# Optimization experiments

Measured on AMD Instinct MI355X. Metric: run time of the kernel, lower is better.

Reference implementation:

```python
import jax, jax.numpy as jnp
import numpy as np

EMBED_DIM = 384
HEADS = 6
HEAD_DIM = EMBED_DIM // HEADS
WINDOW = 64
B, T, M = 256, 256, 128


def setup_inputs() -> dict:
    key = jax.random.key(0)
    ks = jax.random.split(key, 7)
    s = 0.02
    return {
        "x": jax.random.normal(ks[0], (B, T, EMBED_DIM), dtype=jnp.float32),
        "memory": jax.random.normal(ks[1], (M, EMBED_DIM), dtype=jnp.float32),
        "loss_mask": jnp.ones((B, T), dtype=jnp.float32),
        "qkv_w": jax.random.normal(ks[2], (3 * EMBED_DIM, EMBED_DIM), dtype=jnp.float32) * s,
        "qkv_b": jnp.zeros((3 * EMBED_DIM,), dtype=jnp.float32),
        "proj_w": jax.random.normal(ks[3], (EMBED_DIM, EMBED_DIM), dtype=jnp.float32) * s,
        "proj_b": jnp.zeros((EMBED_DIM,), dtype=jnp.float32),
        "gate": jnp.ones((EMBED_DIM,), dtype=jnp.float32),
    }


def reference(x, memory, loss_mask, qkv_w, qkv_b, proj_w, proj_b, gate):
    Bb, Tt, C = x.shape
    H, D, W = HEADS, HEAD_DIM, WINDOW
    Mm = memory.shape[0]
    T_total = Mm + Tt

    qkv = x @ qkv_w.T + qkv_b                     # [B, T, 3C]
    q, k, v = jnp.split(qkv, 3, axis=-1)
    mem = jnp.broadcast_to(memory[None], (Bb, Mm, C))
    k = jnp.concatenate([mem, k], axis=1)          # [B, M+T, C]
    v = jnp.concatenate([mem, v], axis=1)

    q = q.reshape(Bb, Tt, H, D)
    k = k.reshape(Bb, T_total, H, D)
    v = v.reshape(Bb, T_total, H, D)

    att = jnp.einsum('bthd,bshd->bhts', q, k) * (1.0 / np.sqrt(D))  # [B,H,T,M+T]

    # memory prefix columns are fully attended; self-block is causal AND local-window
    i = jnp.arange(Tt)[:, None]
    j = jnp.arange(Tt)[None, :]
    self_mask = (j <= i) & (jnp.abs(i - j) <= W)   # [T, T]
    full_mask = jnp.concatenate(
        [jnp.ones((Tt, Mm), dtype=bool), self_mask], axis=1)  # [T, M+T]
    att = jnp.where(full_mask[None, None], att, -jnp.inf)
    att = jax.nn.softmax(att, axis=-1)

    out = jnp.einsum('bhts,bshd->bthd', att, v).reshape(Bb, Tt, C)
    out = (out * gate) @ proj_w.T + proj_b
    out = out * loss_mask[..., None]
    return out
```

## Files before the change

### kernel.cpp

```cpp
#include <hip/hip_runtime.h>
#include <hip/hip_bf16.h>

#define Bb 256
#define Tt 256
#define Cc 384
#define Hh 6
#define Dd 64
#define Ww 64
#define Mm 128

typedef short short8 __attribute__((ext_vector_type(8)));
typedef float floatx4 __attribute__((ext_vector_type(4)));

static __device__ __forceinline__ unsigned short f2bf(float f) {
  union { __hip_bfloat16 h; unsigned short u; } cvt;
  cvt.h = __float2bfloat16(f);
  return cvt.u;
}

static __device__ __forceinline__ void gl2lds16(const unsigned short* g, unsigned short* l) {
  __builtin_amdgcn_global_load_lds(
      (const __attribute__((address_space(1))) unsigned int*)(const void*)g,
      (__attribute__((address_space(3))) unsigned int*)(void*)l,
      16, 0, 0);
}


__global__ __launch_bounds__(256) void cvt_x(const float4* __restrict__ x,
                                             ushort4* __restrict__ xb) {
  size_t i = (size_t)blockIdx.x * 256 + threadIdx.x;
  float4 v = x[i];
  ushort4 o;
  o.x = f2bf(v.x); o.y = f2bf(v.y); o.z = f2bf(v.z); o.w = f2bf(v.w);
  xb[i] = o;
}

__global__ __launch_bounds__(256) void cvt_misc(const float* __restrict__ qkv_w,
                                                const float* __restrict__ proj_w,
                                                const float* __restrict__ mem,
                                                unsigned short* __restrict__ wb,
                                                unsigned short* __restrict__ pwb,
                                                unsigned short* __restrict__ memk,
                                                unsigned short* __restrict__ memvt) {
  int i = blockIdx.x * 256 + threadIdx.x;
  wb[i] = f2bf(qkv_w[i]);
  if (i < 147456) pwb[i] = f2bf(proj_w[i]);
  if (i < 49152) {
    int m = i / Cc, c = i % Cc, h = c >> 6, d = c & 63;
    unsigned short bv = f2bf(mem[i]);
    memk[(h * Mm + m) * Dd + d] = bv;
    memvt[(h * Dd + d) * Mm + m] = bv;
  }
}


__global__ __launch_bounds__(256) void gemm_qkv(const unsigned short* __restrict__ xb,
                                                const unsigned short* __restrict__ wb,
                                                const float* __restrict__ qkv_b,
                                                unsigned short* __restrict__ q,
                                                unsigned short* __restrict__ k,
                                                unsigned short* __restrict__ vt)
{
  int tid = threadIdx.x;
  int w = tid >> 6, lane = tid & 63, quad = lane >> 4, l16 = lane & 15;

  int orig = blockIdx.y * 9 + blockIdx.x;
  int newid = (orig & 7) * 576 + (orig >> 3);
  int bx = newid % 9, by = newid / 9;

  int rowbase = by * 128;
  int colbase = bx * 128;
  int rowofs = (w >> 1) * 64, colofs = (w & 1) * 64;

  __shared__ __align__(16) unsigned short Alds[2][128 * 32];
  __shared__ __align__(16) unsigned short Blds[2][128 * 32];

  int srow = lane >> 2;
  int skc = (lane & 3) * 8;

#define STAGE_QKV(buf, ks_) do {                                                  \
    int kk = (ks_) * 32;                                                          \
    _Pragma("unroll")                                                             \
    for (int c = w; c < 8; c += 4) {                                              \
      gl2lds16(xb + (size_t)(rowbase + c * 16 + srow) * 384 + kk + skc,           \
               &Alds[buf][c * 512 + lane * 8]);                                   \
      gl2lds16(wb + (size_t)(colbase + c * 16 + srow) * 384 + kk + skc,           \
               &Blds[buf][c * 512 + lane * 8]);                                   \
    }                                                                             \
  } while (0)

#define COMPUTE_QKV(buf) do {                                                     \
    short8 a[4], b[4];                                                            \
    _Pragma("unroll")                                                             \
    for (int rt = 0; rt < 4; ++rt)                                                \
      a[rt] = *reinterpret_cast<const short8*>(                                   \
          &Alds[buf][(rowofs + rt * 16 + l16) * 32 + quad * 8]);                  \
    _Pragma("unroll")                                                             \
    for (int nt = 0; nt < 4; ++nt)                                                \
      b[nt] = *reinterpret_cast<const short8*>(                                   \
          &Blds[buf][(colofs + nt * 16 + l16) * 32 + quad * 8]);                  \
    _Pragma("unroll")                                                             \
    for (int rt = 0; rt < 4; ++rt)                                                \
      _Pragma("unroll")                                                           \
      for (int nt = 0; nt < 4; ++nt)                                              \
        acc[rt][nt] = __builtin_amdgcn_mfma_f32_16x16x32_bf16(a[rt], b[nt],       \
                                                              acc[rt][nt], 0, 0, 0); \
  } while (0)

  floatx4 acc[4][4] = {};
  STAGE_QKV(0, 0);
  __syncthreads();
#pragma unroll
  for (int ks = 0; ks < 12; ks += 2) {
    STAGE_QKV(1, ks + 1);
    COMPUTE_QKV(0);
    __syncthreads();
    if (ks + 2 < 12) STAGE_QKV(0, ks + 2);
    COMPUTE_QKV(1);
    __syncthreads();
  }

#pragma unroll
  for (int nt = 0; nt < 4; ++nt) {
    int col = colbase + colofs + nt * 16 + l16;
    int which = col >= 768 ? 2 : (col >= 384 ? 1 : 0);
    int cc = col - which * 384;
    int h = cc >> 6, d = cc & 63;
    float bias = qkv_b[col];
#pragma unroll
    for (int rt = 0; rt < 4; ++rt) {
#pragma unroll
      for (int r = 0; r < 4; ++r) {
        int row = rowbase + rowofs + rt * 16 + quad * 4 + r;
        int bidx = row >> 8, t = row & 255;
        float val = acc[rt][nt][r] + bias;
        size_t bh = (size_t)bidx * Hh + h;
        if (which == 0) {
          q[(bh * Tt + t) * Dd + d] = f2bf(val * 0.125f);
        } else if (which == 1) {
          k[(bh * Tt + t) * Dd + d] = f2bf(val);
        } else {
          vt[(bh * Dd + d) * Tt + t] = f2bf(val);
        }
      }
    }
  }
#undef STAGE_QKV
#undef COMPUTE_QKV
}

#define PSTRIDE 264

__global__ __launch_bounds__(256, 2) void attn(const unsigned short* __restrict__ q,
                                               const unsigned short* __restrict__ k,
                                               const unsigned short* __restrict__ vt,
                                               const unsigned short* __restrict__ memk,
                                               const unsigned short* __restrict__ memvt,
                                               const float* __restrict__ gate,
                                               unsigned short* __restrict__ aout)
{
  int tq = blockIdx.x, h = blockIdx.y, b = blockIdx.z;
  int t0 = tq * 64;
  int tid = threadIdx.x, w = tid >> 6, lane = tid & 63, quad = lane >> 4, l16 = lane & 15;

  size_t bh = (size_t)b * Hh + h;
  const unsigned short* qp = q + (bh * Tt + t0 + w * 16) * Dd;
  const unsigned short* kp = k + bh * Tt * Dd;
  const unsigned short* vp = vt + bh * Dd * Tt;
  const unsigned short* mkp = memk + (size_t)h * Mm * Dd;
  const unsigned short* mvp = memvt + (size_t)h * Dd * Mm;

  __shared__ __align__(16) unsigned short lds[33280];
  unsigned short* Kmem = lds;
  unsigned short* Kwin = lds + 8192;
  unsigned short* Pb   = lds;
  unsigned short* Vmem = lds + 16896;
  unsigned short* Vwin = lds + 25088;
  unsigned short* pw = Pb + w * 16 * PSTRIDE;

  short8 qa[2];
#pragma unroll
  for (int ks = 0; ks < 2; ++ks)
    qa[ks] = *reinterpret_cast<const short8*>(qp + l16 * Dd + ks * 32 + quad * 8);

#pragma unroll
  for (int i = 0; i < 4; ++i) {
    int G = (i * 4 + w) * 64;
    int g = G + lane;
    int r = g >> 3, cs = g & 7;
    int c = cs ^ (r & 7);
    gl2lds16(mkp + r * 64 + c * 8, Kmem + G * 8 + lane * 8);
  }
#pragma unroll
  for (int i = 0; i < 4; ++i) {
    int G = (i * 4 + w) * 64;
    int g = G + lane;
    int r = g >> 3, cs = g & 7;
    int c = cs ^ (r & 7);
    int j = t0 - 64 + r;
    if (j < 0) j = 0;
    gl2lds16(kp + (size_t)j * 64 + c * 8, Kwin + G * 8 + lane * 8);
  }
#pragma unroll
  for (int i = 0; i < 4; ++i) {
    int G = (i * 4 + w) * 64;
    int g = G + lane;
    int d = g >> 4, cs = g & 15;
    int c = (cs & 8) | ((cs & 7) ^ (d & 7));
    gl2lds16(mvp + d * Mm + c * 8, Vmem + G * 8 + lane * 8);
  }
#pragma unroll
  for (int i = 0; i < 4; ++i) {
    int G = (i * 4 + w) * 64;
    int g = G + lane;
    int d = g >> 4, cs = g & 15;
    int c = (cs & 8) | ((cs & 7) ^ (d & 7));
    int j0 = t0 - 64 + c * 8;
    if (j0 < 0) j0 = 0;
    gl2lds16(vp + (size_t)d * Tt + j0, Vwin + G * 8 + lane * 8);
  }
  __syncthreads();

  floatx4 s[16] = {};

#pragma unroll
  for (int ct = 0; ct < 8; ++ct)
#pragma unroll
    for (int ks = 0; ks < 2; ++ks) {
      int slot = (ks * 4 + quad) ^ (l16 & 7);
      short8 bf = *reinterpret_cast<const short8*>(Kmem + (ct * 16 + l16) * 64 + slot * 8);
      s[ct] = __builtin_amdgcn_mfma_f32_16x16x32_bf16(qa[ks], bf, s[ct], 0, 0, 0);
    }
#pragma unroll
  for (int ct = 0; ct < 8; ++ct) {
    if (ct >= w && ct <= w + 4) {
#pragma unroll
      for (int ks = 0; ks < 2; ++ks) {
        int slot = (ks * 4 + quad) ^ (l16 & 7);
        short8 bf = *reinterpret_cast<const short8*>(Kwin + (ct * 16 + l16) * 64 + slot * 8);
        s[8 + ct] = __builtin_amdgcn_mfma_f32_16x16x32_bf16(qa[ks], bf, s[8 + ct], 0, 0, 0);
      }
    }
  }
  __syncthreads();

#pragma unroll
  for (int ct = 8; ct < 16; ++ct) {
    int j = t0 - 64 + (ct - 8) * 16 + l16;
#pragma unroll
    for (int r = 0; r < 4; ++r) {
      int i = t0 + w * 16 + quad * 4 + r;
      bool valid = (j >= 0) && (j <= i) && (i - j <= 64);
      if (!valid) s[ct][r] = -1e30f;
    }
  }

  float rm[4], rs[4], inv[4];
#pragma unroll
  for (int r = 0; r < 4; ++r) {
    float m = -1e30f;
#pragma unroll
    for (int ct = 0; ct < 16; ++ct) m = fmaxf(m, s[ct][r]);
    rm[r] = m;
  }
#pragma unroll
  for (int off = 1; off < 16; off <<= 1)
#pragma unroll
    for (int r = 0; r < 4; ++r) rm[r] = fmaxf(rm[r], __shfl_xor(rm[r], off, 64));
#pragma unroll
  for (int r = 0; r < 4; ++r) {
    float sum = 0.f;
#pragma unroll
    for (int ct = 0; ct < 16; ++ct) {
      float p = __expf(s[ct][r] - rm[r]);
      s[ct][r] = p;
      sum += p;
    }
    rs[r] = sum;
  }
#pragma unroll
  for (int off = 1; off < 16; off <<= 1)
#pragma unroll
    for (int r = 0; r < 4; ++r) rs[r] += __shfl_xor(rs[r], off, 64);
#pragma unroll
  for (int r = 0; r < 4; ++r) inv[r] = 1.0f / rs[r];

#pragma unroll
  for (int ct = 0; ct < 16; ++ct)
#pragma unroll
    for (int r = 0; r < 4; ++r)
      pw[(quad * 4 + r) * PSTRIDE + ct * 16 + l16] = f2bf(s[ct][r]);

  floatx4 o[4] = {};
#pragma unroll
  for (int ks = 0; ks < 4; ++ks) {
    short8 pa = *reinterpret_cast<const short8*>(pw + l16 * PSTRIDE + ks * 32 + quad * 8);
#pragma unroll
    for (int dt = 0; dt < 4; ++dt) {
      int c0 = ks * 4 + quad;
      int slot = (c0 & 8) | ((c0 & 7) ^ (l16 & 7));
      short8 vb = *reinterpret_cast<const short8*>(Vmem + (dt * 16 + l16) * 128 + slot * 8);
      o[dt] = __builtin_amdgcn_mfma_f32_16x16x32_bf16(pa, vb, o[dt], 0, 0, 0);
    }
  }
#pragma unroll
  for (int ks = 0; ks < 4; ++ks) {
    if (ks >= (w >> 1) && ks <= 2 + (w >> 1)) {
      short8 pa = *reinterpret_cast<const short8*>(pw + l16 * PSTRIDE + (4 + ks) * 32 + quad * 8);
#pragma unroll
      for (int dt = 0; dt < 4; ++dt) {
        int c0 = ks * 4 + quad;
        int slot = (c0 & 8) | ((c0 & 7) ^ (l16 & 7));
        short8 vb = *reinterpret_cast<const short8*>(Vwin + (dt * 16 + l16) * 128 + slot * 8);
        o[dt] = __builtin_amdgcn_mfma_f32_16x16x32_bf16(pa, vb, o[dt], 0, 0, 0);
      }
    }
  }

#pragma unroll
  for (int dt = 0; dt < 4; ++dt) {
    int c = h * 64 + dt * 16 + l16;
    float g = gate[c];
#pragma unroll
    for (int r = 0; r < 4; ++r) {
      int t = t0 + w * 16 + quad * 4 + r;
      float val = o[dt][r] * inv[r] * g;
      aout[((size_t)b * Tt + t) * Cc + c] = f2bf(val);
    }
  }
}


__global__ __launch_bounds__(256) void gemm_proj(const unsigned short* __restrict__ ab,
                                                 const unsigned short* __restrict__ pwb,
                                                 const float* __restrict__ proj_b,
                                                 const float* __restrict__ loss_mask,
                                                 float* __restrict__ out)
{
  int tid = threadIdx.x;
  int w = tid >> 6, lane = tid & 63, quad = lane >> 4, l16 = lane & 15;

  int orig = blockIdx.y * 3 + blockIdx.x;
  int newid = (orig & 7) * 192 + (orig >> 3);
  int bx = newid % 3, by = newid / 3;

  int rowbase = by * 128;
  int colbase = bx * 128;
  int rowofs = (w >> 1) * 64, colofs = (w & 1) * 64;

  __shared__ __align__(16) unsigned short Alds[2][128 * 32];
  __shared__ __align__(16) unsigned short Blds[2][128 * 32];

  int srow = lane >> 2;
  int skc = (lane & 3) * 8;

#define STAGE_PROJ(buf, ks_) do {                                                 \
    int kk = (ks_) * 32;                                                          \
    _Pragma("unroll")                                                             \
    for (int c = w; c < 8; c += 4) {                                              \
      gl2lds16(ab + (size_t)(rowbase + c * 16 + srow) * 384 + kk + skc,           \
               &Alds[buf][c * 512 + lane * 8]);                                   \
      gl2lds16(pwb + (size_t)(colbase + c * 16 + srow) * 384 + kk + skc,          \
               &Blds[buf][c * 512 + lane * 8]);                                   \
    }                                                                             \
  } while (0)

#define COMPUTE_PROJ(buf) do {                                                    \
    short8 a[4], b[4];                                                            \
    _Pragma("unroll")                                                             \
    for (int rt = 0; rt < 4; ++rt)                                                \
      a[rt] = *reinterpret_cast<const short8*>(                                   \
          &Alds[buf][(rowofs + rt * 16 + l16) * 32 + quad * 8]);                  \
    _Pragma("unroll")                                                             \
    for (int nt = 0; nt < 4; ++nt)                                                \
      b[nt] = *reinterpret_cast<const short8*>(                                   \
          &Blds[buf][(colofs + nt * 16 + l16) * 32 + quad * 8]);                  \
    _Pragma("unroll")                                                             \
    for (int rt = 0; rt < 4; ++rt)                                                \
      _Pragma("unroll")                                                           \
      for (int nt = 0; nt < 4; ++nt)                                              \
        acc[rt][nt] = __builtin_amdgcn_mfma_f32_16x16x32_bf16(a[rt], b[nt],       \
                                                              acc[rt][nt], 0, 0, 0); \
  } while (0)

  floatx4 acc[4][4] = {};
  STAGE_PROJ(0, 0);
  __syncthreads();
#pragma unroll
  for (int ks = 0; ks < 12; ks += 2) {
    STAGE_PROJ(1, ks + 1);
    COMPUTE_PROJ(0);
    __syncthreads();
    if (ks + 2 < 12) STAGE_PROJ(0, ks + 2);
    COMPUTE_PROJ(1);
    __syncthreads();
  }

#pragma unroll
  for (int nt = 0; nt < 4; ++nt) {
    int col = colbase + colofs + nt * 16 + l16;
    float bias = proj_b[col];
#pragma unroll
    for (int rt = 0; rt < 4; ++rt) {
#pragma unroll
      for (int r = 0; r < 4; ++r) {
        int row = rowbase + rowofs + rt * 16 + quad * 4 + r;
        float val = (acc[rt][nt][r] + bias) * loss_mask[row];
        out[(size_t)row * 384 + col] = val;
      }
    }
  }
#undef STAGE_PROJ
#undef COMPUTE_PROJ
}


extern "C" void kernel_launch(void* const* d_in, const int* in_sizes, int n_in,
                              void* d_out, int out_size, void* d_ws, size_t ws_size,
                              hipStream_t stream) {
  const float* x = (const float*)d_in[0];
  const float* memory = (const float*)d_in[1];
  const float* loss_mask = (const float*)d_in[2];
  const float* qkv_w = (const float*)d_in[3];
  const float* qkv_b = (const float*)d_in[4];
  const float* proj_w = (const float*)d_in[5];
  const float* proj_b = (const float*)d_in[6];
  const float* gate = (const float*)d_in[7];
  float* out = (float*)d_out;

  char* ws = (char*)d_ws;
  unsigned short* xb    = (unsigned short*)(ws + 0);
  unsigned short* qb    = (unsigned short*)(ws + 50331648);
  unsigned short* kb    = (unsigned short*)(ws + 100663296);
  unsigned short* vtb   = (unsigned short*)(ws + 150994944);
  unsigned short* wb    = (unsigned short*)(ws + 201326592);
  unsigned short* pwb   = (unsigned short*)(ws + 202211328);
  unsigned short* memk  = (unsigned short*)(ws + 202506240);
  unsigned short* memvt = (unsigned short*)(ws + 202604544);
  unsigned short* aout  = xb;

  cvt_x<<<dim3(24576), dim3(256), 0, stream>>>((const float4*)x, (ushort4*)xb);
  cvt_misc<<<dim3(1728), dim3(256), 0, stream>>>(qkv_w, proj_w, memory, wb, pwb, memk, memvt);
  gemm_qkv<<<dim3(9, 512), dim3(256), 0, stream>>>(xb, wb, qkv_b, qb, kb, vtb);
  attn<<<dim3(4, 6, 256), dim3(256), 0, stream>>>(qb, kb, vtb, memk, memvt, gate, aout);
  gemm_proj<<<dim3(3, 512), dim3(256), 0, stream>>>(aout, pwb, proj_b, loss_mask, out);
}
```

Measured before the change: 436.7 us.

## Deepen GEMM K-tiles to 64 with XOR-swizzled LDS and fine-grained vmcnt waits

Both the QKV and projection GEMMs now stage 64-wide K slices instead of 32, which halves the number of pipeline stages and barriers. The LDS layout uses an XOR swizzle to avoid bank conflicts on the wider rows. Full __syncthreads are replaced with explicit s_waitcnt vmcnt plus s_barrier, so the next stage's loads stay in flight while the current one is consumed. MFMA sections are wrapped in s_setprio. The cost is doubled LDS use (64 KB per block), which may reduce occupancy.

```diff
diff --git a/kernel.cpp b/kernel.cpp
--- a/kernel.cpp
+++ b/kernel.cpp
@@ -24,6 +24,9 @@
       (__attribute__((address_space(3))) unsigned int*)(void*)l,
       16, 0, 0);
 }
+
+#define VW(N) asm volatile("s_waitcnt vmcnt(" #N ")" ::: "memory")
+#define BAR() __builtin_amdgcn_s_barrier()
 
 
 __global__ __launch_bounds__(256) void cvt_x(const float4* __restrict__ x,
@@ -72,53 +75,69 @@
   int colbase = bx * 128;
   int rowofs = (w >> 1) * 64, colofs = (w & 1) * 64;
 
-  __shared__ __align__(16) unsigned short Alds[2][128 * 32];
-  __shared__ __align__(16) unsigned short Blds[2][128 * 32];
-
-  int srow = lane >> 2;
-  int skc = (lane & 3) * 8;
-
-#define STAGE_QKV(buf, ks_) do {                                                  \
-    int kk = (ks_) * 32;                                                          \
+  __shared__ __align__(16) unsigned short Alds[2][128 * 64];
+  __shared__ __align__(16) unsigned short Blds[2][128 * 64];
+
+#define STAGE_QKV(buf, s_) do {                                                   \
+    int kk = (s_) * 64;                                                           \
     _Pragma("unroll")                                                             \
-    for (int c = w; c < 8; c += 4) {                                              \
-      gl2lds16(xb + (size_t)(rowbase + c * 16 + srow) * 384 + kk + skc,           \
-               &Alds[buf][c * 512 + lane * 8]);                                   \
-      gl2lds16(wb + (size_t)(colbase + c * 16 + srow) * 384 + kk + skc,           \
-               &Blds[buf][c * 512 + lane * 8]);                                   \
+    for (int i = 0; i < 4; ++i) {                                                 \
+      int g = (i * 4 + w) * 64 + lane;                                            \
+      int r = g >> 3, cs = g & 7, c = cs ^ (r & 7);                               \
+      gl2lds16(xb + (size_t)(rowbase + r) * 384 + kk + c * 8,                     \
+               &Alds[buf][g * 8]);                                                \
+      gl2lds16(wb + (size_t)(colbase + r) * 384 + kk + c * 8,                     \
+               &Blds[buf][g * 8]);                                                \
     }                                                                             \
   } while (0)
 
 #define COMPUTE_QKV(buf) do {                                                     \
-    short8 a[4], b[4];                                                            \
+    __builtin_amdgcn_s_setprio(1);                                                \
     _Pragma("unroll")                                                             \
-    for (int rt = 0; rt < 4; ++rt)                                                \
-      a[rt] = *reinterpret_cast<const short8*>(                                   \
-          &Alds[buf][(rowofs + rt * 16 + l16) * 32 + quad * 8]);                  \
-    _Pragma("unroll")                                                             \
-    for (int nt = 0; nt < 4; ++nt)                                                \
-      b[nt] = *reinterpret_cast<const short8*>(                                   \
-          &Blds[buf][(colofs + nt * 16 + l16) * 32 + quad * 8]);                  \
-    _Pragma("unroll")                                                             \
-    for (int rt = 0; rt < 4; ++rt)                                                \
+    for (int ks = 0; ks < 2; ++ks) {                                              \
+      short8 a[4], b[4];                                                          \
+      int slot = ((ks * 4 + quad) ^ (l16 & 7)) * 8;                               \
+      _Pragma("unroll")                                                           \
+      for (int rt = 0; rt < 4; ++rt)                                              \
+        a[rt] = *reinterpret_cast<const short8*>(                                 \
+            &Alds[buf][(rowofs + rt * 16 + l16) * 64 + slot]);                    \
       _Pragma("unroll")                                                           \
       for (int nt = 0; nt < 4; ++nt)                                              \
-        acc[rt][nt] = __builtin_amdgcn_mfma_f32_16x16x32_bf16(a[rt], b[nt],       \
-                                                              acc[rt][nt], 0, 0, 0); \
+        b[nt] = *reinterpret_cast<const short8*>(                                 \
+            &Blds[buf][(colofs + nt * 16 + l16) * 64 + slot]);                    \
+      _Pragma("unroll")                                                           \
+      for (int rt = 0; rt < 4; ++rt)                                              \
+        _Pragma("unroll")                                                         \
+        for (int nt = 0; nt < 4; ++nt)                                            \
+          acc[rt][nt] = __builtin_amdgcn_mfma_f32_16x16x32_bf16(a[rt], b[nt],     \
+                                                                acc[rt][nt], 0, 0, 0); \
+    }                                                                             \
+    __builtin_amdgcn_s_setprio(0);                                                \
   } while (0)
 
   floatx4 acc[4][4] = {};
   STAGE_QKV(0, 0);
-  __syncthreads();
-#pragma unroll
-  for (int ks = 0; ks < 12; ks += 2) {
-    STAGE_QKV(1, ks + 1);
-    COMPUTE_QKV(0);
-    __syncthreads();
-    if (ks + 2 < 12) STAGE_QKV(0, ks + 2);
-    COMPUTE_QKV(1);
-    __syncthreads();
-  }
+  STAGE_QKV(1, 1);
+  VW(8); BAR();
+  COMPUTE_QKV(0);
+  BAR();
+  STAGE_QKV(0, 2);
+  VW(8); BAR();
+  COMPUTE_QKV(1);
+  BAR();
+  STAGE_QKV(1, 3);
+  VW(8); BAR();
+  COMPUTE_QKV(0);
+  BAR();
+  STAGE_QKV(0, 4);
+  VW(8); BAR();
+  COMPUTE_QKV(1);
+  BAR();
+  STAGE_QKV(1, 5);
+  VW(8); BAR();
+  COMPUTE_QKV(0);
+  VW(0); BAR();
+  COMPUTE_QKV(1);
 
 #pragma unroll
   for (int nt = 0; nt < 4; ++nt) {
@@ -348,53 +367,69 @@
   int colbase = bx * 128;
   int rowofs = (w >> 1) * 64, colofs = (w & 1) * 64;
 
-  __shared__ __align__(16) unsigned short Alds[2][128 * 32];
-  __shared__ __align__(16) unsigned short Blds[2][128 * 32];
-
-  int srow = lane >> 2;
-  int skc = (lane & 3) * 8;
-
-#define STAGE_PROJ(buf, ks_) do {                                                 \
-    int kk = (ks_) * 32;                                                          \
+  __shared__ __align__(16) unsigned short Alds[2][128 * 64];
+  __shared__ __align__(16) unsigned short Blds[2][128 * 64];
+
+#define STAGE_PROJ(buf, s_) do {                                                  \
+    int kk = (s_) * 64;                                                           \
     _Pragma("unroll")                                                             \
-    for (int c = w; c < 8; c += 4) {                                              \
-      gl2lds16(ab + (size_t)(rowbase + c * 16 + srow) * 384 + kk + skc,           \
-               &Alds[buf][c * 512 + lane * 8]);                                   \
-      gl2lds16(pwb + (size_t)(colbase + c * 16 + srow) * 384 + kk + skc,          \
-               &Blds[buf][c * 512 + lane * 8]);                                   \
+    for (int i = 0; i < 4; ++i) {                                                 \
+      int g = (i * 4 + w) * 64 + lane;                                            \
+      int r = g >> 3, cs = g & 7, c = cs ^ (r & 7);                               \
+      gl2lds16(ab + (size_t)(rowbase + r) * 384 + kk + c * 8,                     \
+               &Alds[buf][g * 8]);                                                \
+      gl2lds16(pwb + (size_t)(colbase + r) * 384 + kk + c * 8,                    \
+               &Blds[buf][g * 8]);                                                \
     }                                                                             \
   } while (0)
 
 #define COMPUTE_PROJ(buf) do {                                                    \
-    short8 a[4], b[4];                                                            \
+    __builtin_amdgcn_s_setprio(1);                                                \
     _Pragma("unroll")                                                             \
-    for (int rt = 0; rt < 4; ++rt)                                                \
-      a[rt] = *reinterpret_cast<const short8*>(                                   \
-          &Alds[buf][(rowofs + rt * 16 + l16) * 32 + quad * 8]);                  \
-    _Pragma("unroll")                                                             \
-    for (int nt = 0; nt < 4; ++nt)                                                \
-      b[nt] = *reinterpret_cast<const short8*>(                                   \
-          &Blds[buf][(colofs + nt * 16 + l16) * 32 + quad * 8]);                  \
-    _Pragma("unroll")                                                             \
-    for (int rt = 0; rt < 4; ++rt)                                                \
+    for (int ks = 0; ks < 2; ++ks) {                                              \
+      short8 a[4], b[4];                                                          \
+      int slot = ((ks * 4 + quad) ^ (l16 & 7)) * 8;                               \
+      _Pragma("unroll")                                                           \
+      for (int rt = 0; rt < 4; ++rt)                                              \
+        a[rt] = *reinterpret_cast<const short8*>(                                 \
+            &Alds[buf][(rowofs + rt * 16 + l16) * 64 + slot]);                    \
       _Pragma("unroll")                                                           \
       for (int nt = 0; nt < 4; ++nt)                                              \
-        acc[rt][nt] = __builtin_amdgcn_mfma_f32_16x16x32_bf16(a[rt], b[nt],       \
-                                                              acc[rt][nt], 0, 0, 0); \
+        b[nt] = *reinterpret_cast<const short8*>(                                 \
+            &Blds[buf][(colofs + nt * 16 + l16) * 64 + slot]);                    \
+      _Pragma("unroll")                                                           \
+      for (int rt = 0; rt < 4; ++rt)                                              \
+        _Pragma("unroll")                                                         \
+        for (int nt = 0; nt < 4; ++nt)                                            \
+          acc[rt][nt] = __builtin_amdgcn_mfma_f32_16x16x32_bf16(a[rt], b[nt],     \
+                                                                acc[rt][nt], 0, 0, 0); \
+    }                                                                             \
+    __builtin_amdgcn_s_setprio(0);                                                \
   } while (0)
 
   floatx4 acc[4][4] = {};
   STAGE_PROJ(0, 0);
-  __syncthreads();
-#pragma unroll
-  for (int ks = 0; ks < 12; ks += 2) {
-    STAGE_PROJ(1, ks + 1);
-    COMPUTE_PROJ(0);
-    __syncthreads();
-    if (ks + 2 < 12) STAGE_PROJ(0, ks + 2);
-    COMPUTE_PROJ(1);
-    __syncthreads();
-  }
+  STAGE_PROJ(1, 1);
+  VW(8); BAR();
+  COMPUTE_PROJ(0);
+  BAR();
+  STAGE_PROJ(0, 2);
+  VW(8); BAR();
+  COMPUTE_PROJ(1);
+  BAR();
+  STAGE_PROJ(1, 3);
+  VW(8); BAR();
+  COMPUTE_PROJ(0);
+  BAR();
+  STAGE_PROJ(0, 4);
+  VW(8); BAR();
+  COMPUTE_PROJ(1);
+  BAR();
+  STAGE_PROJ(1, 5);
+  VW(8); BAR();
+  COMPUTE_PROJ(0);
+  VW(0); BAR();
+  COMPUTE_PROJ(1);
 
 #pragma unroll
   for (int nt = 0; nt < 4; ++nt) {
```

Result: faster. 424.5 us (-2.8%).

## Triple-buffer QKV and proj GEMM LDS staging with fine-grained vmcnt waits

Applied to the files above, without the earlier changes.

Both GEMM kernels move from a double-buffered LDS pipeline with __syncthreads to a triple-buffered, fully unrolled schedule that keeps two K-slices in flight and waits with explicit s_waitcnt vmcnt counts plus raw barriers. The LDS layout becomes k-chunk-major (chunk*128 + row), so each lane's 16-byte fragment read is contiguous across l16 and avoids bank conflicts. MFMA blocks are wrapped in s_setprio to favour the matrix issue. Costs are more LDS per block (48KB), which may reduce occupancy, and hand-counted vmcnt values that are fragile if the compiler reorders memory ops.

```diff
diff --git a/kernel.cpp b/kernel.cpp
--- a/kernel.cpp
+++ b/kernel.cpp
@@ -24,6 +24,9 @@
       (__attribute__((address_space(3))) unsigned int*)(void*)l,
       16, 0, 0);
 }
+
+#define VW(N) asm volatile("s_waitcnt vmcnt(" #N ")" ::: "memory")
+#define BAR() __builtin_amdgcn_s_barrier()
 
 
 __global__ __launch_bounds__(256) void cvt_x(const float4* __restrict__ x,
@@ -72,20 +75,19 @@
   int colbase = bx * 128;
   int rowofs = (w >> 1) * 64, colofs = (w & 1) * 64;
 
-  __shared__ __align__(16) unsigned short Alds[2][128 * 32];
-  __shared__ __align__(16) unsigned short Blds[2][128 * 32];
-
-  int srow = lane >> 2;
-  int skc = (lane & 3) * 8;
-
-#define STAGE_QKV(buf, ks_) do {                                                  \
-    int kk = (ks_) * 32;                                                          \
-    _Pragma("unroll")                                                             \
-    for (int c = w; c < 8; c += 4) {                                              \
-      gl2lds16(xb + (size_t)(rowbase + c * 16 + srow) * 384 + kk + skc,           \
-               &Alds[buf][c * 512 + lane * 8]);                                   \
-      gl2lds16(wb + (size_t)(colbase + c * 16 + srow) * 384 + kk + skc,           \
-               &Blds[buf][c * 512 + lane * 8]);                                   \
+  __shared__ __align__(16) unsigned short Alds[3][4096];
+  __shared__ __align__(16) unsigned short Blds[3][4096];
+
+#define STAGE_QKV(buf, s_) do {                                                   \
+    int kk = (s_) * 32;                                                           \
+    _Pragma("unroll")                                                             \
+    for (int i = 0; i < 2; ++i) {                                                 \
+      int g = (i * 4 + w) * 64 + lane;                                            \
+      int r = g & 127, c = g >> 7;                                                \
+      gl2lds16(xb + (size_t)(rowbase + r) * 384 + kk + c * 8,                     \
+               &Alds[buf][g * 8]);                                                \
+      gl2lds16(wb + (size_t)(colbase + r) * 384 + kk + c * 8,                     \
+               &Blds[buf][g * 8]);                                                \
     }                                                                             \
   } while (0)
 
@@ -94,31 +96,38 @@
     _Pragma("unroll")                                                             \
     for (int rt = 0; rt < 4; ++rt)                                                \
       a[rt] = *reinterpret_cast<const short8*>(                                   \
-          &Alds[buf][(rowofs + rt * 16 + l16) * 32 + quad * 8]);                  \
+          &Alds[buf][(quad * 128 + rowofs + rt * 16 + l16) * 8]);                 \
     _Pragma("unroll")                                                             \
     for (int nt = 0; nt < 4; ++nt)                                                \
       b[nt] = *reinterpret_cast<const short8*>(                                   \
-          &Blds[buf][(colofs + nt * 16 + l16) * 32 + quad * 8]);                  \
+          &Blds[buf][(quad * 128 + colofs + nt * 16 + l16) * 8]);                 \
+    __builtin_amdgcn_s_setprio(1);                                                \
     _Pragma("unroll")                                                             \
     for (int rt = 0; rt < 4; ++rt)                                                \
       _Pragma("unroll")                                                           \
       for (int nt = 0; nt < 4; ++nt)                                              \
         acc[rt][nt] = __builtin_amdgcn_mfma_f32_16x16x32_bf16(a[rt], b[nt],       \
                                                               acc[rt][nt], 0, 0, 0); \
+    __builtin_amdgcn_s_setprio(0);                                                \
   } while (0)
 
   floatx4 acc[4][4] = {};
   STAGE_QKV(0, 0);
-  __syncthreads();
-#pragma unroll
-  for (int ks = 0; ks < 12; ks += 2) {
-    STAGE_QKV(1, ks + 1);
-    COMPUTE_QKV(0);
-    __syncthreads();
-    if (ks + 2 < 12) STAGE_QKV(0, ks + 2);
-    COMPUTE_QKV(1);
-    __syncthreads();
-  }
+  STAGE_QKV(1, 1);
+  STAGE_QKV(2, 2);
+  VW(8); BAR();
+  COMPUTE_QKV(0); BAR(); STAGE_QKV(0, 3);  VW(8); BAR();
+  COMPUTE_QKV(1); BAR(); STAGE_QKV(1, 4);  VW(8); BAR();
+  COMPUTE_QKV(2); BAR(); STAGE_QKV(2, 5);  VW(8); BAR();
+  COMPUTE_QKV(0); BAR(); STAGE_QKV(0, 6);  VW(8); BAR();
+  COMPUTE_QKV(1); BAR(); STAGE_QKV(1, 7);  VW(8); BAR();
+  COMPUTE_QKV(2); BAR(); STAGE_QKV(2, 8);  VW(8); BAR();
+  COMPUTE_QKV(0); BAR(); STAGE_QKV(0, 9);  VW(8); BAR();
+  COMPUTE_QKV(1); BAR(); STAGE_QKV(1, 10); VW(8); BAR();
+  COMPUTE_QKV(2); BAR(); STAGE_QKV(2, 11); VW(8); BAR();
+  COMPUTE_QKV(0); BAR(); VW(4); BAR();
+  COMPUTE_QKV(1); VW(0); BAR();
+  COMPUTE_QKV(2);
 
 #pragma unroll
   for (int nt = 0; nt < 4; ++nt) {
@@ -348,20 +357,19 @@
   int colbase = bx * 128;
   int rowofs = (w >> 1) * 64, colofs = (w & 1) * 64;
 
-  __shared__ __align__(16) unsigned short Alds[2][128 * 32];
-  __shared__ __align__(16) unsigned short Blds[2][128 * 32];
-
-  int srow = lane >> 2;
-  int skc = (lane & 3) * 8;
-
-#define STAGE_PROJ(buf, ks_) do {                                                 \
-    int kk = (ks_) * 32;                                                          \
-    _Pragma("unroll")                                                             \
-    for (int c = w; c < 8; c += 4) {                                              \
-      gl2lds16(ab + (size_t)(rowbase + c * 16 + srow) * 384 + kk + skc,           \
-               &Alds[buf][c * 512 + lane * 8]);                                   \
-      gl2lds16(pwb + (size_t)(colbase + c * 16 + srow) * 384 + kk + skc,          \
-               &Blds[buf][c * 512 + lane * 8]);                                   \
+  __shared__ __align__(16) unsigned short Alds[3][4096];
+  __shared__ __align__(16) unsigned short Blds[3][4096];
+
+#define STAGE_PROJ(buf, s_) do {                                                  \
+    int kk = (s_) * 32;                                                           \
+    _Pragma("unroll")                                                             \
+    for (int i = 0; i < 2; ++i) {                                                 \
+      int g = (i * 4 + w) * 64 + lane;                                            \
+      int r = g & 127, c = g >> 7;                                                \
+      gl2lds16(ab + (size_t)(rowbase + r) * 384 + kk + c * 8,                     \
+               &Alds[buf][g * 8]);                                                \
+      gl2lds16(pwb + (size_t)(colbase + r) * 384 + kk + c * 8,                    \
+               &Blds[buf][g * 8]);                                                \
     }                                                                             \
   } while (0)
 
@@ -370,31 +378,38 @@
     _Pragma("unroll")                                                             \
     for (int rt = 0; rt < 4; ++rt)                                                \
       a[rt] = *reinterpret_cast<const short8*>(                                   \
-          &Alds[buf][(rowofs + rt * 16 + l16) * 32 + quad * 8]);                  \
+          &Alds[buf][(quad * 128 + rowofs + rt * 16 + l16) * 8]);                 \
     _Pragma("unroll")                                                             \
     for (int nt = 0; nt < 4; ++nt)                                                \
       b[nt] = *reinterpret_cast<const short8*>(                                   \
-          &Blds[buf][(colofs + nt * 16 + l16) * 32 + quad * 8]);                  \
+          &Blds[buf][(quad * 128 + colofs + nt * 16 + l16) * 8]);                 \
+    __builtin_amdgcn_s_setprio(1);                                                \
     _Pragma("unroll")                                                             \
     for (int rt = 0; rt < 4; ++rt)                                                \
       _Pragma("unroll")                                                           \
       for (int nt = 0; nt < 4; ++nt)                                              \
         acc[rt][nt] = __builtin_amdgcn_mfma_f32_16x16x32_bf16(a[rt], b[nt],       \
                                                               acc[rt][nt], 0, 0, 0); \
+    __builtin_amdgcn_s_setprio(0);                                                \
   } while (0)
 
   floatx4 acc[4][4] = {};
   STAGE_PROJ(0, 0);
-  __syncthreads();
-#pragma unroll
-  for (int ks = 0; ks < 12; ks += 2) {
-    STAGE_PROJ(1, ks + 1);
-    COMPUTE_PROJ(0);
-    __syncthreads();
-    if (ks + 2 < 12) STAGE_PROJ(0, ks + 2);
-    COMPUTE_PROJ(1);
-    __syncthreads();
-  }
+  STAGE_PROJ(1, 1);
+  STAGE_PROJ(2, 2);
+  VW(8); BAR();
+  COMPUTE_PROJ(0); BAR(); STAGE_PROJ(0, 3);  VW(8); BAR();
+  COMPUTE_PROJ(1); BAR(); STAGE_PROJ(1, 4);  VW(8); BAR();
+  COMPUTE_PROJ(2); BAR(); STAGE_PROJ(2, 5);  VW(8); BAR();
+  COMPUTE_PROJ(0); BAR(); STAGE_PROJ(0, 6);  VW(8); BAR();
+  COMPUTE_PROJ(1); BAR(); STAGE_PROJ(1, 7);  VW(8); BAR();
+  COMPUTE_PROJ(2); BAR(); STAGE_PROJ(2, 8);  VW(8); BAR();
+  COMPUTE_PROJ(0); BAR(); STAGE_PROJ(0, 9);  VW(8); BAR();
+  COMPUTE_PROJ(1); BAR(); STAGE_PROJ(1, 10); VW(8); BAR();
+  COMPUTE_PROJ(2); BAR(); STAGE_PROJ(2, 11); VW(8); BAR();
+  COMPUTE_PROJ(0); BAR(); VW(4); BAR();
+  COMPUTE_PROJ(1); VW(0); BAR();
+  COMPUTE_PROJ(2);
 
 #pragma unroll
   for (int nt = 0; nt < 4; ++nt) {
```

Measured after the change: 495.9 us. +13.6%, slower.
